# Optimization experiments

Measured on AMD Instinct MI355X. Metric: run time of the kernel, lower is better.

Reference implementation:

```python
import jax, jax.numpy as jnp
import numpy as np

NFEATS = 768; NHIDS = 768; H = 8; HD = NHIDS // H
NT = 32768; NC = 32768; NS = 32768; DEG = 8; E = NT * DEG
ALPHA = 0.2  # LeakyReLU negative slope


def setup_inputs() -> dict:
    key = jax.random.key(0)
    ks = jax.random.split(key, 16)
    f32 = jnp.float32
    dst = jnp.repeat(jnp.arange(NT, dtype=jnp.int32), DEG)  # uniform in-degree mailbox
    return {
        'h': jax.random.normal(ks[0], (NT, NFEATS), f32),
        'hb_c_src': jax.random.normal(ks[1], (NC, NHIDS), f32),
        'hb_s_src': jax.random.normal(ks[2], (NS, NHIDS), f32),
        'Wg': jax.random.normal(ks[3], (H, NFEATS, HD), f32) * 0.05,
        'bg': jnp.zeros((H, HD), f32),
        'ag': jax.random.normal(ks[4], (H, 2 * HD), f32) * 0.1,
        'agb': jnp.zeros((H,), f32),
        'Wx': jax.random.normal(ks[5], (H, NHIDS, HD), f32) * 0.05,
        'bx': jnp.zeros((H, HD), f32),
        'ax': jax.random.normal(ks[6], (H, 2 * HD), f32) * 0.1,
        'axb': jnp.zeros((H,), f32),
        'Wih': jax.random.normal(ks[7], (3 * NHIDS, NHIDS), f32) * 0.02,
        'Whh': jax.random.normal(ks[8], (3 * NHIDS, NHIDS), f32) * 0.02,
        'bih': jnp.zeros((3 * NHIDS,), f32),
        'bhh': jnp.zeros((3 * NHIDS,), f32),
        'intra_src': jax.random.randint(ks[9], (E,), 0, NT, jnp.int32),
        'intra_dst': dst,
        'c_src': jax.random.randint(ks[10], (E,), 0, NC, jnp.int32),
        'c_dst': dst,
        's_src': jax.random.randint(ks[11], (E,), 0, NS, jnp.int32),
        's_dst': dst,
    }


def _attend(Wh_s, Wh_d, src, dst, a, ab, n_dst):
    """Multi-head GAT edge attention + segment softmax + weighted aggregation.
    Wh_s: [Ns,H,D] src projections, Wh_d: [Nd,H,D] dst projections.
    a([Wh_src||Wh_dst]) decomposed as a_src.Wh_src + a_dst.Wh_dst + bias."""
    D = Wh_s.shape[-1]
    e = (jnp.einsum('nhd,hd->nh', Wh_s, a[:, :D])[src]
         + jnp.einsum('nhd,hd->nh', Wh_d, a[:, D:])[dst] + ab)  # [E,H]
    e = jax.nn.leaky_relu(e, ALPHA)
    m = jax.ops.segment_max(e, dst, num_segments=n_dst)
    ex = jnp.exp(e - m[dst])
    den = jax.ops.segment_sum(ex, dst, num_segments=n_dst)
    att = ex / den[dst]  # per-dst softmax over incoming edges (DGL mailbox softmax)
    out = jax.ops.segment_sum(Wh_s[src] * att[..., None], dst, num_segments=n_dst)
    return out.reshape(n_dst, H * D)  # concat heads


def _forward(h, hb_c_src, hb_s_src, Wg, bg, ag, agb, Wx, bx, ax, axb,
             Wih, Whh, bih, bhh, intra_src, intra_dst, c_src, c_dst, s_src, s_dst):
    n = h.shape[0]
    # intra-turn GAT (x = self.gat(g, t)); dropout is identity in eval mode
    Wh = jnp.einsum('nf,hfd->nhd', h, Wg) + bg
    x = _attend(Wh, Wh, intra_src, intra_dst, ag, agb, n)
    # cross-turn inversed GAT; dst nodes' 'hb' feature is the fresh gat output x;
    # counter_bw and support_bw share the same xgat weights.
    Wx_d = jnp.einsum('nf,hfd->nhd', x, Wx) + bx
    Wc_s = jnp.einsum('nf,hfd->nhd', hb_c_src, Wx) + bx
    h_c = _attend(Wc_s, Wx_d, c_src, c_dst, ax, axb, n)
    Ws_s = jnp.einsum('nf,hfd->nhd', hb_s_src, Wx) + bx
    h_s = _attend(Ws_s, Wx_d, s_src, s_dst, ax, axb, n)
    hid = 0.5 * h_c + 0.5 * h_s
    # GRUCell(x, hid)
    gi = x @ Wih.T + bih
    gh = hid @ Whh.T + bhh
    ir, iz, inn = jnp.split(gi, 3, axis=1)
    hr, hz, hn = jnp.split(gh, 3, axis=1)
    r = jax.nn.sigmoid(ir + hr)
    z = jax.nn.sigmoid(iz + hz)
    cand = jnp.tanh(inn + r * hn)
    return (1.0 - z) * cand + z * hid


def reference(h, hb_c_src, hb_s_src, Wg, bg, ag, agb, Wx, bx, ax, axb,
              Wih, Whh, bih, bhh, intra_src, intra_dst, c_src, c_dst, s_src, s_dst):
    return _forward(h, hb_c_src, hb_s_src, Wg, bg, ag, agb, Wx, bx, ax, axb,
                    Wih, Whh, bih, bhh, intra_src, intra_dst, c_src, c_dst, s_src, s_dst)
```

## Files before the change

### kernel.cpp

```cpp
#include <hip/hip_runtime.h>
#include <hip/hip_bf16.h>
#include <math.h>

#define NT 32768
#define HD 96
#define DEG 8
#define NE (NT * DEG)
#define LRELU_ALPHA 0.2f
#define CH 16384

typedef __attribute__((ext_vector_type(8))) short bf16x8;
typedef __attribute__((ext_vector_type(8))) unsigned short u16x8;
typedef __attribute__((ext_vector_type(4))) unsigned short u16x4;
typedef __attribute__((ext_vector_type(4))) float f32x4;

__device__ __forceinline__ unsigned short f2bf(float x) {
    union { float f; unsigned u; } v; v.f = x;
    unsigned r = v.u + 0x7FFFu + ((v.u >> 16) & 1u);
    return (unsigned short)(r >> 16);
}
__device__ __forceinline__ float bf2f(unsigned short u) {
    union { unsigned u; float f; } v; v.u = ((unsigned)u) << 16; return v.f;
}

__device__ __forceinline__ void gload_lds16(const void* g, void* l) {
    __builtin_amdgcn_global_load_lds(
        (const __attribute__((address_space(1))) void*)g,
        (__attribute__((address_space(3))) void*)l, 16, 0, 0);
}


__global__ void packWT(const float* __restrict__ W, unsigned short* __restrict__ T) {
    int idx = blockIdx.x * 256 + threadIdx.x;
    if (idx >= 768 * 768) return;
    int c = idx / 768, f = idx % 768;
    T[idx] = f2bf(W[(size_t)(c / HD) * 768 * HD + (size_t)f * HD + (c % HD)]);
}

__global__ void cvt_bf8(const float* __restrict__ X, unsigned short* __restrict__ Y, int n8) {
    int i = blockIdx.x * 256 + threadIdx.x;
    if (i >= n8) return;
    float4 a = ((const float4*)X)[2 * i];
    float4 b = ((const float4*)X)[2 * i + 1];
    u16x8 p;
    p[0] = f2bf(a.x); p[1] = f2bf(a.y); p[2] = f2bf(a.z); p[3] = f2bf(a.w);
    p[4] = f2bf(b.x); p[5] = f2bf(b.y); p[6] = f2bf(b.z); p[7] = f2bf(b.w);
    ((u16x8*)Y)[i] = p;
}

__global__ void packWV(const float* __restrict__ Wx, const float* __restrict__ ax,
                       const float* __restrict__ bx,
                       float* __restrict__ wv, float* __restrict__ cd) {
    int idx = blockIdx.x * 256 + threadIdx.x;
    if (idx < 8 * 768) {
        int h = idx / 768, f = idx % 768;
        const float* wp = Wx + (size_t)h * 768 * HD + (size_t)f * HD;
        const float* ap = ax + h * 2 * HD + HD;
        float s = 0.f;
        for (int d = 0; d < HD; d++) s += wp[d] * ap[d];
        wv[idx] = s;
    }
    if (idx < 8) {
        const float* bp = bx + idx * HD;
        const float* ap = ax + idx * 2 * HD + HD;
        float s = 0.f;
        for (int d = 0; d < HD; d++) s += bp[d] * ap[d];
        cd[idx] = s;
    }
}

__global__ __launch_bounds__(512, 2) void mgemm3(
    const unsigned short* __restrict__ A1, const unsigned short* __restrict__ A2,
    const unsigned short* __restrict__ BT1, const unsigned short* __restrict__ BT2,
    const float* __restrict__ bias1, const float* __restrict__ bias2,
    unsigned short* __restrict__ C1, unsigned short* __restrict__ C2,
    int mt1, int N, int K) {
    __shared__ unsigned short Alds[2][256 * 64];
    __shared__ unsigned short Blds[2][256 * 64];
    const int tid = threadIdx.x;
    const int w = tid >> 6, l = tid & 63;
    const int wr = w >> 2, wc = w & 3;
    const int lrow = l & 15, lk = l >> 4;

    const int nx = gridDim.x;
    const int nwg = nx * gridDim.y;
    int lin = blockIdx.y * nx + blockIdx.x;
    if ((nwg & 7) == 0) lin = (lin & 7) * (nwg >> 3) + (lin >> 3);
    int bm = lin / nx;
    const int bn = lin % nx;

    const bool p1 = bm < mt1;
    const unsigned short* A  = p1 ? A1 : A2;
    const unsigned short* BT = p1 ? BT1 : BT2;
    const float* bias        = p1 ? bias1 : bias2;
    unsigned short* C        = p1 ? C1 : C2;
    if (!p1) bm -= mt1;

    const unsigned short* asrc[4];
    const unsigned short* bsrc[4];
    #pragma unroll
    for (int q = 0; q < 4; q++) {
        int idx = q * 512 + tid;
        int r = idx >> 3, s = idx & 7;
        int kw = s ^ ((r >> 1) & 7);
        asrc[q] = A  + (size_t)(bm * 256 + r) * K + kw * 8;
        bsrc[q] = BT + (size_t)(bn * 256 + r) * K + kw * 8;
    }
    const int ldst = w * 512;

    f32x4 acc[8][4] = {};
    const int nt = K >> 6;

    #pragma unroll
    for (int q = 0; q < 4; q++) {
        gload_lds16(asrc[q], &Alds[0][q * 4096 + ldst]);
        gload_lds16(bsrc[q], &Blds[0][q * 4096 + ldst]);
    }

    for (int t = 0; t < nt; ++t) {
        const int cur = t & 1;
        __syncthreads();
        if (t + 1 < nt) {
            const int k1 = (t + 1) << 6;
            #pragma unroll
            for (int q = 0; q < 4; q++) {
                gload_lds16(asrc[q] + k1, &Alds[cur ^ 1][q * 4096 + ldst]);
                gload_lds16(bsrc[q] + k1, &Blds[cur ^ 1][q * 4096 + ldst]);
            }
        }
        #pragma unroll
        for (int ks = 0; ks < 2; ks++) {
            bf16x8 bfv[4], af[8];
            #pragma unroll
            for (int j = 0; j < 4; j++) {
                int r = wc * 64 + j * 16 + lrow;
                int s = (ks * 4 + lk) ^ ((r >> 1) & 7);
                bfv[j] = *(const bf16x8*)(&Blds[cur][r * 64 + s * 8]);
            }
            #pragma unroll
            for (int i = 0; i < 8; i++) {
                int r = wr * 128 + i * 16 + lrow;
                int s = (ks * 4 + lk) ^ ((r >> 1) & 7);
                af[i] = *(const bf16x8*)(&Alds[cur][r * 64 + s * 8]);
            }
            __builtin_amdgcn_s_setprio(1);
            #pragma unroll
            for (int i = 0; i < 8; i++)
                #pragma unroll
                for (int j = 0; j < 4; j++)
                    acc[i][j] = __builtin_amdgcn_mfma_f32_16x16x32_bf16(af[i], bfv[j], acc[i][j], 0, 0, 0);
            __builtin_amdgcn_s_setprio(0);
        }
    }

    const size_t crow0 = (size_t)bm * 256 + wr * 128;
    const int ccol0 = bn * 256 + wc * 64;
    #pragma unroll
    for (int j = 0; j < 4; j++) {
        int col = ccol0 + j * 16 + lrow;
        float bv = bias[col];
        #pragma unroll
        for (int i = 0; i < 8; i++) {
            size_t row = crow0 + i * 16 + lk * 4;
            #pragma unroll
            for (int e = 0; e < 4; e++)
                C[(row + e) * N + col] = f2bf(acc[i][j][e] + bv);
        }
    }
}

__global__ __launch_bounds__(256) void escore2(
    const unsigned short* __restrict__ X, const float* __restrict__ a,
    float* __restrict__ s0out, float* __restrict__ s1out) {
    __shared__ float av0[768], av1[768];
    for (int t = threadIdx.x; t < 768; t += 256) {
        int hh = t / HD, d = t % HD;
        av0[t] = a[hh * 2 * HD + d];
        av1[t] = a[hh * 2 * HD + HD + d];
    }
    __syncthreads();
    int idx = blockIdx.x * 256 + threadIdx.x;
    int row = idx >> 3, hh = idx & 7;
    const unsigned short* xp = X + (size_t)row * 768 + hh * HD;
    const float* a0 = av0 + hh * HD;
    const float* a1 = av1 + hh * HD;
    float s0 = 0.f, s1 = 0.f;
    #pragma unroll
    for (int q = 0; q < 12; q++) {
        u16x8 v = *(const u16x8*)(xp + q * 8);
        #pragma unroll
        for (int e = 0; e < 8; e++) {
            float x = bf2f(v[e]);
            s0 += x * a0[q * 8 + e];
            s1 += x * a1[q * 8 + e];
        }
    }
    s0out[idx] = s0;
    s1out[idx] = s1;
}

__global__ __launch_bounds__(256) void escore(
    const unsigned short* __restrict__ X, const float* __restrict__ a,
    int half, float* __restrict__ sc) {
    __shared__ float av[768];
    for (int t = threadIdx.x; t < 768; t += 256) {
        int hh = t / HD, d = t % HD;
        av[t] = a[hh * 2 * HD + half * HD + d];
    }
    __syncthreads();
    int idx = blockIdx.x * 256 + threadIdx.x;
    int row = idx >> 3, hh = idx & 7;
    const unsigned short* xp = X + (size_t)row * 768 + hh * HD;
    const float* ap = av + hh * HD;
    float s = 0.f;
    #pragma unroll
    for (int q = 0; q < 12; q++) {
        u16x8 v = *(const u16x8*)(xp + q * 8);
        #pragma unroll
        for (int e = 0; e < 8; e++) s += bf2f(v[e]) * ap[q * 8 + e];
    }
    sc[idx] = s;
}

__global__ __launch_bounds__(256) void escore_fold(
    const unsigned short* __restrict__ X, const float* __restrict__ wv,
    const float* __restrict__ cd, float* __restrict__ ed) {
    __shared__ float wvs[8][8][97];
    __shared__ float cds[8];
    for (int i = threadIdx.x; i < 8 * 8 * 96; i += 256) {
        int j = i / (8 * 96); int r = i % (8 * 96); int h = r / 96; int t = r % 96;
        wvs[j][h][t] = wv[h * 768 + j * 96 + t];
    }
    if (threadIdx.x < 8) cds[threadIdx.x] = cd[threadIdx.x];
    __syncthreads();
    int idx = blockIdx.x * 256 + threadIdx.x;
    int n = idx >> 3, j = idx & 7;
    const unsigned short* xp = X + (size_t)n * 768 + j * 96;
    float p[8] = {};
    #pragma unroll
    for (int q = 0; q < 12; q++) {
        u16x8 v = *(const u16x8*)(xp + q * 8);
        #pragma unroll
        for (int e = 0; e < 8; e++) {
            float x = bf2f(v[e]);
            #pragma unroll
            for (int h = 0; h < 8; h++) p[h] += x * wvs[j][h][q * 8 + e];
        }
    }
    #pragma unroll
    for (int o = 1; o < 8; o <<= 1)
        #pragma unroll
        for (int h = 0; h < 8; h++) p[h] += __shfl_xor(p[h], o, 64);
    ed[(size_t)n * 8 + j] = p[j] + cds[j];
}

__global__ __launch_bounds__(256) void attend_agg(
    const unsigned short* __restrict__ Whs, const float* __restrict__ es,
    const float* __restrict__ ed, const float* __restrict__ ab,
    const int* __restrict__ src, const int* __restrict__ dst,
    unsigned short* __restrict__ out) {
    const int wv = threadIdx.x >> 6, l = threadIdx.x & 63;
    const int seg = blockIdx.x * 4 + wv;
    const int hh = l >> 3, j = l & 7;
    int sj = src[seg * 8 + j];
    int dnode = dst[seg * 8];
    float e = es[(size_t)sj * 8 + hh] + ed[(size_t)dnode * 8 + hh] + ab[hh];
    e = e > 0.f ? e : LRELU_ALPHA * e;
    float m = e;
    #pragma unroll
    for (int o = 1; o < 8; o <<= 1) m = fmaxf(m, __shfl_xor(m, o, 64));
    float ex = expf(e - m);
    float s = ex;
    #pragma unroll
    for (int o = 1; o < 8; o <<= 1) s += __shfl_xor(s, o, 64);
    float att = ex / s;

    #pragma unroll
    for (int u = 0; u < 3; u++) {
        int c = 4 * l + 256 * u;
        int h = c / HD;
        float acc0 = 0.f, acc1 = 0.f, acc2 = 0.f, acc3 = 0.f;
        #pragma unroll
        for (int j2 = 0; j2 < 8; j2++) {
            float a = __shfl(att, h * 8 + j2, 64);
            int sid = __shfl(sj, j2, 64);
            u16x4 v = *(const u16x4*)(Whs + (size_t)sid * 768 + c);
            acc0 += a * bf2f(v[0]); acc1 += a * bf2f(v[1]);
            acc2 += a * bf2f(v[2]); acc3 += a * bf2f(v[3]);
        }
        u16x4 r;
        r[0] = f2bf(acc0); r[1] = f2bf(acc1); r[2] = f2bf(acc2); r[3] = f2bf(acc3);
        *(u16x4*)(out + (size_t)dnode * 768 + c) = r;
    }
}

__global__ __launch_bounds__(256) void attend2(
    const unsigned short* __restrict__ Wc, const unsigned short* __restrict__ Ws,
    const float* __restrict__ esC, const float* __restrict__ esS,
    const float* __restrict__ ed, const float* __restrict__ ab,
    const int* __restrict__ csrc, const int* __restrict__ ssrc,
    const int* __restrict__ dst, unsigned short* __restrict__ outH) {
    const int wv = threadIdx.x >> 6, l = threadIdx.x & 63;
    const int seg = blockIdx.x * 4 + wv;
    const int hh = l >> 3, j = l & 7;
    int cj = csrc[seg * 8 + j];
    int sj = ssrc[seg * 8 + j];
    int dnode = dst[seg * 8];
    float edv = ed[(size_t)dnode * 8 + hh] + ab[hh];

    float eC = esC[(size_t)cj * 8 + hh] + edv;
    eC = eC > 0.f ? eC : LRELU_ALPHA * eC;
    float mC = eC;
    #pragma unroll
    for (int o = 1; o < 8; o <<= 1) mC = fmaxf(mC, __shfl_xor(mC, o, 64));
    float exC = expf(eC - mC);
    float sC = exC;
    #pragma unroll
    for (int o = 1; o < 8; o <<= 1) sC += __shfl_xor(sC, o, 64);
    float attC = exC / sC;

    float eS = esS[(size_t)sj * 8 + hh] + edv;
    eS = eS > 0.f ? eS : LRELU_ALPHA * eS;
    float mS = eS;
    #pragma unroll
    for (int o = 1; o < 8; o <<= 1) mS = fmaxf(mS, __shfl_xor(mS, o, 64));
    float exS = expf(eS - mS);
    float sS = exS;
    #pragma unroll
    for (int o = 1; o < 8; o <<= 1) sS += __shfl_xor(sS, o, 64);
    float attS = exS / sS;

    #pragma unroll
    for (int u = 0; u < 3; u++) {
        int c = 4 * l + 256 * u;
        int h = c / HD;
        float acc0 = 0.f, acc1 = 0.f, acc2 = 0.f, acc3 = 0.f;
        #pragma unroll
        for (int j2 = 0; j2 < 8; j2++) {
            float a = __shfl(attC, h * 8 + j2, 64);
            int sid = __shfl(cj, j2, 64);
            u16x4 v = *(const u16x4*)(Wc + (size_t)sid * 768 + c);
            acc0 += a * bf2f(v[0]); acc1 += a * bf2f(v[1]);
            acc2 += a * bf2f(v[2]); acc3 += a * bf2f(v[3]);
        }
        #pragma unroll
        for (int j2 = 0; j2 < 8; j2++) {
            float a = __shfl(attS, h * 8 + j2, 64);
            int sid = __shfl(sj, j2, 64);
            u16x4 v = *(const u16x4*)(Ws + (size_t)sid * 768 + c);
            acc0 += a * bf2f(v[0]); acc1 += a * bf2f(v[1]);
            acc2 += a * bf2f(v[2]); acc3 += a * bf2f(v[3]);
        }
        u16x4 r;
        r[0] = f2bf(0.5f * acc0); r[1] = f2bf(0.5f * acc1);
        r[2] = f2bf(0.5f * acc2); r[3] = f2bf(0.5f * acc3);
        *(u16x4*)(outH + (size_t)dnode * 768 + c) = r;
    }
}

__global__ __launch_bounds__(256) void gru_elem(
    const unsigned short* __restrict__ gi, const unsigned short* __restrict__ gh,
    const unsigned short* __restrict__ hid, float* __restrict__ out) {
    int idx = blockIdx.x * 256 + threadIdx.x;
    int nrow = idx / 96, c8 = (idx % 96) * 8;
    const unsigned short* gip = gi + (size_t)nrow * 2304 + c8;
    const unsigned short* ghp = gh + (size_t)nrow * 2304 + c8;
    u16x8 vir = *(const u16x8*)(gip);
    u16x8 viz = *(const u16x8*)(gip + 768);
    u16x8 vin = *(const u16x8*)(gip + 1536);
    u16x8 vhr = *(const u16x8*)(ghp);
    u16x8 vhz = *(const u16x8*)(ghp + 768);
    u16x8 vhn = *(const u16x8*)(ghp + 1536);
    u16x8 vh  = *(const u16x8*)(hid + (size_t)nrow * 768 + c8);
    float res[8];
    #pragma unroll
    for (int e = 0; e < 8; e++) {
        float r = 1.f / (1.f + expf(-(bf2f(vir[e]) + bf2f(vhr[e]))));
        float z = 1.f / (1.f + expf(-(bf2f(viz[e]) + bf2f(vhz[e]))));
        float cand = tanhf(bf2f(vin[e]) + r * bf2f(vhn[e]));
        res[e] = (1.f - z) * cand + z * bf2f(vh[e]);
    }
    float* op = out + (size_t)nrow * 768 + c8;
    *(float4*)(op)     = make_float4(res[0], res[1], res[2], res[3]);
    *(float4*)(op + 4) = make_float4(res[4], res[5], res[6], res[7]);
}

extern "C" void kernel_launch(void* const* d_in, const int* in_sizes, int n_in,
                              void* d_out, int out_size, void* d_ws, size_t ws_size,
                              hipStream_t stream) {
    const float* h    = (const float*)d_in[0];
    const float* hbc  = (const float*)d_in[1];
    const float* hbs  = (const float*)d_in[2];
    const float* Wg   = (const float*)d_in[3];
    const float* bg   = (const float*)d_in[4];
    const float* ag   = (const float*)d_in[5];
    const float* agb  = (const float*)d_in[6];
    const float* Wx   = (const float*)d_in[7];
    const float* bx   = (const float*)d_in[8];
    const float* ax   = (const float*)d_in[9];
    const float* axb  = (const float*)d_in[10];
    const float* Wih  = (const float*)d_in[11];
    const float* Whh  = (const float*)d_in[12];
    const float* bih  = (const float*)d_in[13];
    const float* bhh  = (const float*)d_in[14];
    const int* i_src  = (const int*)d_in[15];
    const int* i_dst  = (const int*)d_in[16];
    const int* c_src  = (const int*)d_in[17];
    const int* c_dst  = (const int*)d_in[18];
    const int* s_src  = (const int*)d_in[19];
    const int* s_dst  = (const int*)d_in[20];
    float* out = (float*)d_out;

    const size_t SZ = (size_t)NT * 768;
    unsigned short* Xb   = (unsigned short*)d_ws;
    unsigned short* Hdb  = Xb + SZ;
    unsigned short* GIb  = Hdb + SZ;
    unsigned short* GHb  = GIb + (size_t)CH * 2304;
    unsigned short* ABh  = GIb;
    unsigned short* ABc  = GIb + SZ;
    unsigned short* ABs  = GIb + 2 * SZ;
    unsigned short* W2gT = GHb + (size_t)CH * 2304;
    unsigned short* W2xT = W2gT + 768 * 768;
    unsigned short* WihB = W2xT + 768 * 768;
    unsigned short* WhhB = WihB + 2304 * 768;
    float* EScat = (float*)(WhhB + 2304 * 768);
    float* ED    = EScat + 2 * NE;
    float* ESI   = ED + NE;
    float* EDI   = ESI + NE;
    float* WV    = EDI + NE;
    float* CD    = WV + 8 * 768;
    unsigned short* Pcat = (unsigned short*)d_out;

    dim3 blk(256);
    dim3 blk512(512);
    packWT<<<(768 * 768 + 255) / 256, blk, 0, stream>>>(Wg, W2gT);
    packWT<<<(768 * 768 + 255) / 256, blk, 0, stream>>>(Wx, W2xT);
    cvt_bf8<<<(2304 * 768 / 8 + 255) / 256, blk, 0, stream>>>(Wih, WihB, 2304 * 768 / 8);
    cvt_bf8<<<(2304 * 768 / 8 + 255) / 256, blk, 0, stream>>>(Whh, WhhB, 2304 * 768 / 8);
    packWV<<<(8 * 768 + 255) / 256, blk, 0, stream>>>(Wx, ax, bx, WV, CD);

    const int n8 = (int)(SZ / 8);
    const int cvtg = (n8 + 255) / 256;

    cvt_bf8<<<cvtg, blk, 0, stream>>>(h,   ABh, n8);
    cvt_bf8<<<cvtg, blk, 0, stream>>>(hbc, ABc, n8);
    cvt_bf8<<<cvtg, blk, 0, stream>>>(hbs, ABs, n8);

    dim3 gproj(3, 384);
    mgemm3<<<gproj, blk512, 0, stream>>>(ABh, ABc, W2gT, W2xT, bg, bx,
                                         Hdb, Pcat, 128, 768, 768);
    escore2<<<NE / 256, blk, 0, stream>>>(Hdb, ag, ESI, EDI);
    attend_agg<<<NT / 4, blk, 0, stream>>>(Hdb, ESI, EDI, agb, i_src, i_dst, Xb);
    escore_fold<<<NE / 256, blk, 0, stream>>>(Xb, WV, CD, ED);
    escore<<<2 * NE / 256, blk, 0, stream>>>(Pcat, ax, 0, EScat);
    attend2<<<NT / 4, blk, 0, stream>>>(Pcat, Pcat + SZ, EScat, EScat + NE, ED, axb,
                                        c_src, s_src, c_dst, Hdb);
    dim3 ggru(9, 128);
    for (int c0 = 0; c0 < NT; c0 += CH) {
        mgemm3<<<ggru, blk512, 0, stream>>>(Xb + (size_t)c0 * 768, Hdb + (size_t)c0 * 768,
                                            WihB, WhhB, bih, bhh, GIb, GHb,
                                            64, 2304, 768);
        gru_elem<<<(CH * 96) / 256, blk, 0, stream>>>(GIb, GHb, Hdb + (size_t)c0 * 768, out + (size_t)c0 * 768);
    }
}
```

Baseline: 990.9 us.

## Restructure bf16 GEMM mainloop into 8-wave split-K ping-pong pipeline

```diff
diff --git a/kernel.cpp b/kernel.cpp
--- a/kernel.cpp
+++ b/kernel.cpp
@@ -69,14 +69,14 @@
     }
 }
 
-__global__ __launch_bounds__(512, 2) void mgemm3(
+__global__ __launch_bounds__(512, 2) void mgemm8(
     const unsigned short* __restrict__ A1, const unsigned short* __restrict__ A2,
     const unsigned short* __restrict__ BT1, const unsigned short* __restrict__ BT2,
     const float* __restrict__ bias1, const float* __restrict__ bias2,
     unsigned short* __restrict__ C1, unsigned short* __restrict__ C2,
     int mt1, int N, int K) {
-    __shared__ unsigned short Alds[2][256 * 64];
-    __shared__ unsigned short Blds[2][256 * 64];
+    __shared__ unsigned short Al[2][2][256 * 32];
+    __shared__ unsigned short Bl[2][2][256 * 32];
     const int tid = threadIdx.x;
     const int w = tid >> 6, l = tid & 63;
     const int wr = w >> 2, wc = w & 3;
@@ -96,61 +96,93 @@
     unsigned short* C        = p1 ? C1 : C2;
     if (!p1) bm -= mt1;
 
-    const unsigned short* asrc[4];
-    const unsigned short* bsrc[4];
-    #pragma unroll
-    for (int q = 0; q < 4; q++) {
-        int idx = q * 512 + tid;
-        int r = idx >> 3, s = idx & 7;
-        int kw = s ^ ((r >> 1) & 7);
-        asrc[q] = A  + (size_t)(bm * 256 + r) * K + kw * 8;
-        bsrc[q] = BT + (size_t)(bn * 256 + r) * K + kw * 8;
-    }
-    const int ldst = w * 512;
+    const int r_loc = tid >> 2;
+    const int s2    = tid & 3;
+    const int kwz   = s2 ^ ((r_loc >> 1) & 3);
+    const unsigned short* aBase = A  + ((size_t)bm * 256 + r_loc) * K + kwz * 8;
+    const unsigned short* bBase = BT + ((size_t)bn * 256 + r_loc) * K + kwz * 8;
+    const int wrow = w * 16;
+
+    const int nkt = K >> 6;
+
+    auto stageA = [&](int kt, int kh) {
+        const int buf = kt & 1;
+        const size_t koff = (size_t)kt * 64 + kh * 32;
+        gload_lds16(aBase + koff,                   &Al[buf][kh][(0   + wrow) * 32]);
+        gload_lds16(aBase + (size_t)128 * K + koff, &Al[buf][kh][(128 + wrow) * 32]);
+    };
+    auto stageB = [&](int kt, int kh) {
+        const int buf = kt & 1;
+        const size_t koff = (size_t)kt * 64 + kh * 32;
+        gload_lds16(bBase + koff,                   &Bl[buf][kh][(0   + wrow) * 32]);
+        gload_lds16(bBase + (size_t)128 * K + koff, &Bl[buf][kh][(128 + wrow) * 32]);
+    };
+    auto ldA = [&](int buf, int ks, int ih, bf16x8* af) {
+        #pragma unroll
+        for (int i = 0; i < 4; i++) {
+            int r = wr * 128 + ih * 64 + i * 16 + lrow;
+            int s = lk ^ ((r >> 1) & 3);
+            af[i] = *(const bf16x8*)(&Al[buf][ks][r * 32 + s * 8]);
+        }
+    };
+    auto ldB = [&](int buf, int ks, bf16x8* bv) {
+        #pragma unroll
+        for (int j = 0; j < 4; j++) {
+            int r = wc * 64 + j * 16 + lrow;
+            int s = lk ^ ((r >> 1) & 3);
+            bv[j] = *(const bf16x8*)(&Bl[buf][ks][r * 32 + s * 8]);
+        }
+    };
 
     f32x4 acc[8][4] = {};
-    const int nt = K >> 6;
-
-    #pragma unroll
-    for (int q = 0; q < 4; q++) {
-        gload_lds16(asrc[q], &Alds[0][q * 4096 + ldst]);
-        gload_lds16(bsrc[q], &Blds[0][q * 4096 + ldst]);
-    }
-
-    for (int t = 0; t < nt; ++t) {
-        const int cur = t & 1;
-        __syncthreads();
-        if (t + 1 < nt) {
-            const int k1 = (t + 1) << 6;
+    auto MM = [&](int ih, bf16x8* af, bf16x8* bv) {
+        __builtin_amdgcn_s_setprio(1);
+        #pragma unroll
+        for (int i = 0; i < 4; i++)
             #pragma unroll
-            for (int q = 0; q < 4; q++) {
-                gload_lds16(asrc[q] + k1, &Alds[cur ^ 1][q * 4096 + ldst]);
-                gload_lds16(bsrc[q] + k1, &Blds[cur ^ 1][q * 4096 + ldst]);
-            }
-        }
-        #pragma unroll
-        for (int ks = 0; ks < 2; ks++) {
-            bf16x8 bfv[4], af[8];
-            #pragma unroll
-            for (int j = 0; j < 4; j++) {
-                int r = wc * 64 + j * 16 + lrow;
-                int s = (ks * 4 + lk) ^ ((r >> 1) & 7);
-                bfv[j] = *(const bf16x8*)(&Blds[cur][r * 64 + s * 8]);
-            }
-            #pragma unroll
-            for (int i = 0; i < 8; i++) {
-                int r = wr * 128 + i * 16 + lrow;
-                int s = (ks * 4 + lk) ^ ((r >> 1) & 7);
-                af[i] = *(const bf16x8*)(&Alds[cur][r * 64 + s * 8]);
-            }
-            __builtin_amdgcn_s_setprio(1);
-            #pragma unroll
-            for (int i = 0; i < 8; i++)
-                #pragma unroll
-                for (int j = 0; j < 4; j++)
-                    acc[i][j] = __builtin_amdgcn_mfma_f32_16x16x32_bf16(af[i], bfv[j], acc[i][j], 0, 0, 0);
-            __builtin_amdgcn_s_setprio(0);
-        }
+            for (int j = 0; j < 4; j++)
+                acc[ih * 4 + i][j] = __builtin_amdgcn_mfma_f32_16x16x32_bf16(
+                    af[i], bv[j], acc[ih * 4 + i][j], 0, 0, 0);
+        __builtin_amdgcn_s_setprio(0);
+    };
+
+    stageA(0, 0); stageB(0, 0);
+    stageA(0, 1); stageB(0, 1);
+    if (nkt > 1) { stageA(1, 0); stageB(1, 0); }
+    asm volatile("s_waitcnt vmcnt(8)" ::: "memory");
+    __builtin_amdgcn_sched_barrier(0);
+    __builtin_amdgcn_s_barrier();
+
+    for (int kt = 0; kt < nkt; ++kt) {
+        const int buf = kt & 1;
+        bf16x8 af[4], bv0[4], bv1[4];
+        ldB(buf, 0, bv0); ldA(buf, 0, 0, af);
+        if (kt + 1 < nkt) stageA(kt + 1, 1);
+        __builtin_amdgcn_s_barrier();
+        MM(0, af, bv0);
+        __builtin_amdgcn_s_barrier();
+        ldA(buf, 0, 1, af);
+        if (kt + 1 < nkt) stageB(kt + 1, 1);
+        __builtin_amdgcn_s_barrier();
+        MM(1, af, bv0);
+        if (kt < nkt - 1) { asm volatile("s_waitcnt vmcnt(8)" ::: "memory"); }
+        else              { asm volatile("s_waitcnt vmcnt(0)" ::: "memory"); }
+        __builtin_amdgcn_sched_barrier(0);
+        __builtin_amdgcn_s_barrier();
+        ldB(buf, 1, bv1); ldA(buf, 1, 0, af);
+        if (kt + 2 < nkt) { stageA(kt + 2, 0); stageB(kt + 2, 0); }
+        __builtin_amdgcn_s_barrier();
+        MM(0, af, bv1);
+        __builtin_amdgcn_s_barrier();
+        ldA(buf, 1, 1, af);
+        __builtin_amdgcn_s_barrier();
+        MM(1, af, bv1);
+        if (kt + 1 < nkt) {
+            if (kt + 1 < nkt - 1) { asm volatile("s_waitcnt vmcnt(8)" ::: "memory"); }
+            else                  { asm volatile("s_waitcnt vmcnt(4)" ::: "memory"); }
+            __builtin_amdgcn_sched_barrier(0);
+        }
+        __builtin_amdgcn_s_barrier();
     }
 
     const size_t crow0 = (size_t)bm * 256 + wr * 128;
@@ -447,7 +479,7 @@
     cvt_bf8<<<cvtg, blk, 0, stream>>>(hbs, ABs, n8);
 
     dim3 gproj(3, 384);
-    mgemm3<<<gproj, blk512, 0, stream>>>(ABh, ABc, W2gT, W2xT, bg, bx,
+    mgemm8<<<gproj, blk512, 0, stream>>>(ABh, ABc, W2gT, W2xT, bg, bx,
                                          Hdb, Pcat, 128, 768, 768);
     escore2<<<NE / 256, blk, 0, stream>>>(Hdb, ag, ESI, EDI);
     attend_agg<<<NT / 4, blk, 0, stream>>>(Hdb, ESI, EDI, agb, i_src, i_dst, Xb);
@@ -457,7 +489,7 @@
                                         c_src, s_src, c_dst, Hdb);
     dim3 ggru(9, 128);
     for (int c0 = 0; c0 < NT; c0 += CH) {
-        mgemm3<<<ggru, blk512, 0, stream>>>(Xb + (size_t)c0 * 768, Hdb + (size_t)c0 * 768,
+        mgemm8<<<ggru, blk512, 0, stream>>>(Xb + (size_t)c0 * 768, Hdb + (size_t)c0 * 768,
                                             WihB, WhhB, bih, bhh, GIb, GHb,
                                             64, 2304, 768);
         gru_elem<<<(CH * 96) / 256, blk, 0, stream>>>(GIb, GHb, Hdb + (size_t)c0 * 768, out + (size_t)c0 * 768);
```

Result: no change. 979.8 us (-1.1%).
